# Kernel tuning notes

Hardware: AMD Instinct MI355X
Metric: run time of the kernel (lower is better)

## Reference

```python
import jax, jax.numpy as jnp
import numpy as np

N = 50000      # nodes
E = 500000     # edges (includes N self-loops)
DIN = 512
DOUT = 256
NEG_SLOPE = 0.01  # torch nn.LeakyReLU default


def setup_inputs() -> dict:
    key = jax.random.key(0)
    k1, k2, k3, k4, k5 = jax.random.split(key, 5)
    x = jax.random.normal(k1, (N, DIN), dtype=jnp.float32)
    # xavier_normal_ with gain=1.414
    std_W = 1.414 * np.sqrt(2.0 / (DIN + DOUT))
    W = jax.random.normal(k2, (DIN, DOUT), dtype=jnp.float32) * std_W
    std_a = 1.414 * np.sqrt(2.0 / (1 + 2 * DOUT))
    a = jax.random.normal(k3, (2 * DOUT,), dtype=jnp.float32) * std_a
    # first N edges are self-loops so every row-sum is nonzero
    loops = jnp.arange(N, dtype=jnp.int32)
    edge_src = jnp.concatenate([loops, jax.random.randint(k4, (E - N,), 0, N, dtype=jnp.int32)])
    edge_dst = jnp.concatenate([loops, jax.random.randint(k5, (E - N,), 0, N, dtype=jnp.int32)])
    return {"x": x, "W": W, "a": a, "edge_src": edge_src, "edge_dst": edge_dst}


def reference(x, W, a, edge_src, edge_dst):
    n = x.shape[0]
    d = W.shape[1]
    h = x @ W  # [N, DOUT]
    # a . [h_src ; h_dst] decomposed per-node, then gathered per-edge
    s_src = h @ a[:d]   # [N]
    s_dst = h @ a[d:]   # [N]
    score = s_src[edge_src] + s_dst[edge_dst]          # [E]
    e = jnp.exp(-jax.nn.leaky_relu(score, NEG_SLOPE))  # [E]
    # sparse softmax denominator: spmm(edge, e, ones) == segment sum over src
    e_rowsum = jax.ops.segment_sum(e, edge_src, num_segments=n)            # [N]
    # numerator: spmm(edge, e, h) == sum_j e_ij * h_j per row i
    h_prime = jax.ops.segment_sum(e[:, None] * h[edge_dst], edge_src, num_segments=n)  # [N, DOUT]
    h_prime = h_prime / e_rowsum[:, None]
    return jax.nn.elu(h_prime)  # concat=True branch
```

## Files before the change

### kernel.cpp

```cpp
#include <hip/hip_runtime.h>
#include <math.h>

#define DIN 512
#define DOUT 256
#define NEG_SLOPE 0.01f

typedef __attribute__((ext_vector_type(8))) short bf16x8;
typedef __attribute__((ext_vector_type(4))) float f32x4;
typedef __attribute__((ext_vector_type(4))) unsigned int u32x4;

__device__ __forceinline__ unsigned short f2bf(float f) {
    unsigned int u = __float_as_uint(f);
    unsigned int r = (u + 0x7FFFu + ((u >> 16) & 1u)) >> 16;
    return (unsigned short)r;
}
__device__ __forceinline__ float bf2f(unsigned short u) {
    return __uint_as_float(((unsigned int)u) << 16);
}
__device__ __forceinline__ unsigned int cvtpk(float lo, float hi) {
    unsigned int r;
    asm("v_cvt_pk_bf16_f32 %0, %1, %2" : "=v"(r) : "v"(lo), "v"(hi));
    return r;
}

__global__ void prep(const float* __restrict__ W, unsigned short* __restrict__ Bp,
                     int* __restrict__ deg, float* __restrict__ s_src,
                     float* __restrict__ s_dst, int N) {
    int t = blockIdx.x * blockDim.x + threadIdx.x;
    if (t < (DIN / 32) * (DOUT / 16) * 64) {
        int lane = t & 63;
        int cg = (t >> 6) & 15;
        int ks = t >> 10;
        int l15 = lane & 15, g = lane >> 4;
        int col = cg * 16 + l15;
        int k0 = ks * 32 + g * 8;
        ushort4 lo, hi;
        lo.x = f2bf(W[(size_t)(k0 + 0) * DOUT + col]);
        lo.y = f2bf(W[(size_t)(k0 + 1) * DOUT + col]);
        lo.z = f2bf(W[(size_t)(k0 + 2) * DOUT + col]);
        lo.w = f2bf(W[(size_t)(k0 + 3) * DOUT + col]);
        hi.x = f2bf(W[(size_t)(k0 + 4) * DOUT + col]);
        hi.y = f2bf(W[(size_t)(k0 + 5) * DOUT + col]);
        hi.z = f2bf(W[(size_t)(k0 + 6) * DOUT + col]);
        hi.w = f2bf(W[(size_t)(k0 + 7) * DOUT + col]);
        *(ushort4*)(Bp + (size_t)t * 8) = lo;
        *(ushort4*)(Bp + (size_t)t * 8 + 4) = hi;
    }
    if (t < N) { deg[t] = 0; s_src[t] = 0.f; s_dst[t] = 0.f; }
}

__global__ __launch_bounds__(256, 4) void gemm_k(const float* __restrict__ x,
                                                 const unsigned short* __restrict__ Bp,
                                                 unsigned short* __restrict__ hb,
                                                 const float* __restrict__ av,
                                                 float* __restrict__ s_src,
                                                 float* __restrict__ s_dst, int M) {
    const int t = threadIdx.x;
    const int lane = t & 63;
    const int l15 = lane & 15;
    const int g = lane >> 4;
    const int wv = t >> 6;
    const int m0 = blockIdx.x * 32;

    f32x4 acc[2][4] = {};
    int r0 = min(m0 + l15, M - 1);
    int r1 = min(m0 + 16 + l15, M - 1);
    const float* pA0 = x + (size_t)r0 * DIN + g * 8;
    const float* pA1 = x + (size_t)r1 * DIN + g * 8;
    const unsigned short* pB = Bp + ((size_t)(wv * 4) * 64 + lane) * 8;

#pragma unroll 4
    for (int ks = 0; ks < DIN / 32; ++ks) {
        f32x4 v0 = *(const f32x4*)(pA0 + ks * 32);
        f32x4 v1 = *(const f32x4*)(pA0 + ks * 32 + 4);
        f32x4 w0 = *(const f32x4*)(pA1 + ks * 32);
        f32x4 w1 = *(const f32x4*)(pA1 + ks * 32 + 4);
        u32x4 p;
        p.x = cvtpk(v0.x, v0.y); p.y = cvtpk(v0.z, v0.w);
        p.z = cvtpk(v1.x, v1.y); p.w = cvtpk(v1.z, v1.w);
        bf16x8 afr0 = *(bf16x8*)&p;
        u32x4 q;
        q.x = cvtpk(w0.x, w0.y); q.y = cvtpk(w0.z, w0.w);
        q.z = cvtpk(w1.x, w1.y); q.w = cvtpk(w1.z, w1.w);
        bf16x8 afr1 = *(bf16x8*)&q;
#pragma unroll
        for (int cf = 0; cf < 4; ++cf) {
            bf16x8 bfr = *(const bf16x8*)(pB + ((size_t)(ks * 16 + cf) * 64) * 8);
            acc[0][cf] = __builtin_amdgcn_mfma_f32_16x16x32_bf16(afr0, bfr, acc[0][cf], 0, 0, 0);
            acc[1][cf] = __builtin_amdgcn_mfma_f32_16x16x32_bf16(afr1, bfr, acc[1][cf], 0, 0, 0);
        }
    }

    float as_[4], ad_[4];
#pragma unroll
    for (int cf = 0; cf < 4; ++cf) {
        int col = wv * 64 + cf * 16 + l15;
        as_[cf] = av[col];
        ad_[cf] = av[DOUT + col];
    }
#pragma unroll
    for (int rf = 0; rf < 2; ++rf) {
#pragma unroll
        for (int j = 0; j < 4; ++j) {
            int row = m0 + rf * 16 + g * 4 + j;
            float ps = 0.f, pd = 0.f;
#pragma unroll
            for (int cf = 0; cf < 4; ++cf) {
                float v = acc[rf][cf][j];
                ps += v * as_[cf];
                pd += v * ad_[cf];
            }
#pragma unroll
            for (int off = 1; off < 16; off <<= 1) {
                ps += __shfl_xor(ps, off);
                pd += __shfl_xor(pd, off);
            }
            if (row < M) {
#pragma unroll
                for (int cf = 0; cf < 4; ++cf)
                    hb[(size_t)row * DOUT + wv * 64 + cf * 16 + l15] = f2bf(acc[rf][cf][j]);
                if (l15 == 0) {
                    atomicAdd(&s_src[row], ps);
                    atomicAdd(&s_dst[row], pd);
                }
            }
        }
    }
}

__global__ void hist_k(const int* __restrict__ src, int* __restrict__ deg, int E) {
    int i = blockIdx.x * blockDim.x + threadIdx.x;
    if (i < E) atomicAdd(&deg[src[i]], 1);
}

__global__ __launch_bounds__(256) void block_sum(const int* __restrict__ deg, int* __restrict__ bsum, int N) {
    __shared__ int wsum[4];
    int b = blockIdx.x, t = threadIdx.x;
    int idx = b * 1024 + t * 4;
    int s = 0;
    if (idx + 3 < N) {
        int4 v = *(const int4*)(deg + idx);
        s = v.x + v.y + v.z + v.w;
    } else {
        for (int i = 0; i < 4; i++) if (idx + i < N) s += deg[idx + i];
    }
#pragma unroll
    for (int off = 32; off > 0; off >>= 1) s += __shfl_xor(s, off);
    if ((t & 63) == 0) wsum[t >> 6] = s;
    __syncthreads();
    if (t == 0) bsum[b] = wsum[0] + wsum[1] + wsum[2] + wsum[3];
}

__global__ void scan_tops(const int* __restrict__ bsum, int* __restrict__ boff,
                          int* __restrict__ rowptr, int nb, int N, int E) {
    int t = threadIdx.x;
    int v = (t < nb) ? bsum[t] : 0;
    int x = v;
#pragma unroll
    for (int off = 1; off < 64; off <<= 1) {
        int y = __shfl_up(x, off);
        if (t >= off) x += y;
    }
    if (t < nb) boff[t] = x - v;
    if (t == 0) rowptr[N] = E;
}

__global__ __launch_bounds__(256) void scan_blk(const int* __restrict__ deg, const int* __restrict__ boff,
                                                int* __restrict__ rowptr, int* __restrict__ cursor, int N) {
    __shared__ int wsum[4];
    int b = blockIdx.x, t = threadIdx.x;
    int idx = b * 1024 + t * 4;
    int v0 = 0, v1 = 0, v2 = 0, v3 = 0;
    if (idx + 3 < N) {
        int4 v = *(const int4*)(deg + idx);
        v0 = v.x; v1 = v.y; v2 = v.z; v3 = v.w;
    } else if (idx < N) {
        v0 = deg[idx];
        if (idx + 1 < N) v1 = deg[idx + 1];
        if (idx + 2 < N) v2 = deg[idx + 2];
    }
    int s = v0 + v1 + v2 + v3;
    int lane = t & 63, wid = t >> 6;
    int x = s;
#pragma unroll
    for (int off = 1; off < 64; off <<= 1) {
        int y = __shfl_up(x, off);
        if (lane >= off) x += y;
    }
    if (lane == 63) wsum[wid] = x;
    __syncthreads();
    int add = boff[b];
    for (int ww = 0; ww < wid; ++ww) add += wsum[ww];
    int e0 = add + x - s;
    int e1 = e0 + v0, e2 = e1 + v1, e3 = e2 + v2;
    if (idx < N)     { rowptr[idx] = e0;     cursor[idx] = e0; }
    if (idx + 1 < N) { rowptr[idx + 1] = e1; cursor[idx + 1] = e1; }
    if (idx + 2 < N) { rowptr[idx + 2] = e2; cursor[idx + 2] = e2; }
    if (idx + 3 < N) { rowptr[idx + 3] = e3; cursor[idx + 3] = e3; }
}

__global__ void edge_k(const int* __restrict__ src, const int* __restrict__ dst,
                       const float* __restrict__ s_src, const float* __restrict__ s_dst,
                       int* __restrict__ cursor, int2* __restrict__ csr, int E) {
    int i = blockIdx.x * blockDim.x + threadIdx.x;
    if (i >= E) return;
    int s = src[i], d = dst[i];
    float sc = s_src[s] + s_dst[d];
    float lrv = sc > 0.f ? sc : NEG_SLOPE * sc;
    float ev = __expf(-lrv);
    int pos = atomicAdd(&cursor[s], 1);
    csr[pos] = make_int2(d, __float_as_int(ev));
}

__global__ __launch_bounds__(256) void gather_k(const unsigned short* __restrict__ hb,
                                                const int* __restrict__ rowptr,
                                                const int2* __restrict__ csr,
                                                float* __restrict__ out, int N) {
    int gt = blockIdx.x * blockDim.x + threadIdx.x;
    int w = gt >> 6;
    int lane = threadIdx.x & 63;
    if (w >= N) return;
    int s0 = rowptr[w], s1 = rowptr[w + 1];
    float a0 = 0.f, a1 = 0.f, a2 = 0.f, a3 = 0.f, rs = 0.f;
    for (int base = s0; base < s1; base += 64) {
        int cnt = min(64, s1 - base);
        int dv = 0; float ev = 0.f;
        if (lane < cnt) {
            int2 p = csr[base + lane];
            dv = p.x; ev = __int_as_float(p.y);
        }
        int jj = 0;
        for (; jj + 4 <= cnt; jj += 4) {
            int d0 = __shfl(dv, jj), d1 = __shfl(dv, jj + 1), d2 = __shfl(dv, jj + 2), d3 = __shfl(dv, jj + 3);
            float e0 = __shfl(ev, jj), e1 = __shfl(ev, jj + 1), e2 = __shfl(ev, jj + 2), e3 = __shfl(ev, jj + 3);
            ushort4 h0 = *(const ushort4*)(hb + (size_t)d0 * DOUT + lane * 4);
            ushort4 h1 = *(const ushort4*)(hb + (size_t)d1 * DOUT + lane * 4);
            ushort4 h2 = *(const ushort4*)(hb + (size_t)d2 * DOUT + lane * 4);
            ushort4 h3 = *(const ushort4*)(hb + (size_t)d3 * DOUT + lane * 4);
            a0 += e0 * bf2f(h0.x) + e1 * bf2f(h1.x) + e2 * bf2f(h2.x) + e3 * bf2f(h3.x);
            a1 += e0 * bf2f(h0.y) + e1 * bf2f(h1.y) + e2 * bf2f(h2.y) + e3 * bf2f(h3.y);
            a2 += e0 * bf2f(h0.z) + e1 * bf2f(h1.z) + e2 * bf2f(h2.z) + e3 * bf2f(h3.z);
            a3 += e0 * bf2f(h0.w) + e1 * bf2f(h1.w) + e2 * bf2f(h2.w) + e3 * bf2f(h3.w);
            rs += e0 + e1 + e2 + e3;
        }
        for (; jj < cnt; ++jj) {
            int d0 = __shfl(dv, jj);
            float e0 = __shfl(ev, jj);
            ushort4 h0 = *(const ushort4*)(hb + (size_t)d0 * DOUT + lane * 4);
            a0 += e0 * bf2f(h0.x);
            a1 += e0 * bf2f(h0.y);
            a2 += e0 * bf2f(h0.z);
            a3 += e0 * bf2f(h0.w);
            rs += e0;
        }
    }
    float inv = 1.f / rs;
    float4 v;
    v.x = a0 * inv; v.y = a1 * inv; v.z = a2 * inv; v.w = a3 * inv;
    v.x = v.x > 0.f ? v.x : __expf(v.x) - 1.f;
    v.y = v.y > 0.f ? v.y : __expf(v.y) - 1.f;
    v.z = v.z > 0.f ? v.z : __expf(v.z) - 1.f;
    v.w = v.w > 0.f ? v.w : __expf(v.w) - 1.f;
    *(float4*)(out + (size_t)w * DOUT + lane * 4) = v;
}

extern "C" void kernel_launch(void* const* d_in, const int* in_sizes, int n_in,
                              void* d_out, int out_size, void* d_ws, size_t ws_size,
                              hipStream_t stream) {
    const float* x = (const float*)d_in[0];
    const float* W = (const float*)d_in[1];
    const float* a = (const float*)d_in[2];
    const int* edge_src = (const int*)d_in[3];
    const int* edge_dst = (const int*)d_in[4];

    const int N = in_sizes[0] / DIN;
    const int E = in_sizes[3];
    const int nb = (N + 1023) / 1024;

    char* ws = (char*)d_ws;
    size_t off = 0;
    auto alloc = [&](size_t bytes) {
        void* p = ws + off;
        off += (bytes + 15) & ~(size_t)15;
        return p;
    };
    unsigned short* hb = (unsigned short*)alloc((size_t)N * DOUT * 2);
    unsigned short* Bp = (unsigned short*)alloc((size_t)DIN * DOUT * 2);
    int* rowptr = (int*)alloc((size_t)(N + 1) * 4);
    int* deg = (int*)alloc((size_t)N * 4);
    int* cursor = (int*)alloc((size_t)N * 4);
    float* s_src = (float*)alloc((size_t)N * 4);
    float* s_dst = (float*)alloc((size_t)N * 4);
    int2* csr = (int2*)alloc((size_t)E * 8);
    int* bsum = (int*)alloc((size_t)nb * 4);
    int* boff = (int*)alloc((size_t)nb * 4);
    (void)ws_size;

    float* out = (float*)d_out;

    prep<<<(N + 255) / 256, 256, 0, stream>>>(W, Bp, deg, s_src, s_dst, N);
    hist_k<<<(E + 255) / 256, 256, 0, stream>>>(edge_src, deg, E);
    gemm_k<<<(N + 31) / 32, 256, 0, stream>>>(x, Bp, hb, a, s_src, s_dst, N);
    block_sum<<<nb, 256, 0, stream>>>(deg, bsum, N);
    scan_tops<<<1, 64, 0, stream>>>(bsum, boff, rowptr, nb, N, E);
    scan_blk<<<nb, 256, 0, stream>>>(deg, boff, rowptr, cursor, N);
    edge_k<<<(E + 255) / 256, 256, 0, stream>>>(edge_src, edge_dst, s_src, s_dst,
                                                cursor, csr, E);
    gather_k<<<(N + 3) / 4, 256, 0, stream>>>(hb, rowptr, csr, out, N);
}
```

Measured before the change: 178.7 us.

## Give each GEMM wave full output width over 16 rows with bulk A prefetch

The GEMM tiling changes from four waves sharing 32 rows, each owning 64 output columns, to each wave owning 16 rows across all 256 columns. Each block now covers 64 rows. Each wave reads its x rows exactly once, loaded in two large batches of sixteen 16-byte loads, so the second half streams in while the first half's MFMAs run. This removes the 4x redundant reads of x across waves but reads all of the packed W per wave. It also raises register use (16 accumulators plus 16 raw vectors), and the occupancy hint is dropped from launch bounds.

```diff
diff --git a/kernel.cpp b/kernel.cpp
--- a/kernel.cpp
+++ b/kernel.cpp
@@ -49,80 +49,106 @@
     if (t < N) { deg[t] = 0; s_src[t] = 0.f; s_dst[t] = 0.f; }
 }
 
-__global__ __launch_bounds__(256, 4) void gemm_k(const float* __restrict__ x,
-                                                 const unsigned short* __restrict__ Bp,
-                                                 unsigned short* __restrict__ hb,
-                                                 const float* __restrict__ av,
-                                                 float* __restrict__ s_src,
-                                                 float* __restrict__ s_dst, int M) {
+__global__ __launch_bounds__(256) void gemm_k(const float* __restrict__ x,
+                                              const unsigned short* __restrict__ Bp,
+                                              unsigned short* __restrict__ hb,
+                                              const float* __restrict__ av,
+                                              float* __restrict__ s_src,
+                                              float* __restrict__ s_dst, int M) {
     const int t = threadIdx.x;
     const int lane = t & 63;
     const int l15 = lane & 15;
     const int g = lane >> 4;
     const int wv = t >> 6;
-    const int m0 = blockIdx.x * 32;
-
-    f32x4 acc[2][4] = {};
-    int r0 = min(m0 + l15, M - 1);
-    int r1 = min(m0 + 16 + l15, M - 1);
-    const float* pA0 = x + (size_t)r0 * DIN + g * 8;
-    const float* pA1 = x + (size_t)r1 * DIN + g * 8;
-    const unsigned short* pB = Bp + ((size_t)(wv * 4) * 64 + lane) * 8;
-
-#pragma unroll 4
-    for (int ks = 0; ks < DIN / 32; ++ks) {
-        f32x4 v0 = *(const f32x4*)(pA0 + ks * 32);
-        f32x4 v1 = *(const f32x4*)(pA0 + ks * 32 + 4);
-        f32x4 w0 = *(const f32x4*)(pA1 + ks * 32);
-        f32x4 w1 = *(const f32x4*)(pA1 + ks * 32 + 4);
+    const int m0 = blockIdx.x * 64 + wv * 16;
+
+    int r = min(m0 + l15, M - 1);
+    const float* pA = x + (size_t)r * DIN + g * 8;
+    const unsigned short* pB = Bp + (size_t)lane * 8;
+
+    f32x4 acc[16] = {};
+    bf16x8 afr[8];
+
+    {
+        f32x4 raw[16];
+#pragma unroll
+        for (int i = 0; i < 8; ++i) {
+            raw[2 * i] = *(const f32x4*)(pA + i * 32);
+            raw[2 * i + 1] = *(const f32x4*)(pA + i * 32 + 4);
+        }
+#pragma unroll
+        for (int i = 0; i < 8; ++i) {
+            u32x4 p;
+            p.x = cvtpk(raw[2 * i].x, raw[2 * i].y);
+            p.y = cvtpk(raw[2 * i].z, raw[2 * i].w);
+            p.z = cvtpk(raw[2 * i + 1].x, raw[2 * i + 1].y);
+            p.w = cvtpk(raw[2 * i + 1].z, raw[2 * i + 1].w);
+            afr[i] = *(bf16x8*)&p;
+        }
+    }
+    f32x4 raw2[16];
+#pragma unroll
+    for (int i = 0; i < 8; ++i) {
+        raw2[2 * i] = *(const f32x4*)(pA + 256 + i * 32);
+        raw2[2 * i + 1] = *(const f32x4*)(pA + 256 + i * 32 + 4);
+    }
+#pragma unroll
+    for (int ks = 0; ks < 8; ++ks) {
+        const unsigned short* pBks = pB + (size_t)ks * 16 * 512;
+#pragma unroll
+        for (int cg = 0; cg < 16; ++cg) {
+            bf16x8 bfr = *(const bf16x8*)(pBks + (size_t)cg * 512);
+            acc[cg] = __builtin_amdgcn_mfma_f32_16x16x32_bf16(afr[ks], bfr, acc[cg], 0, 0, 0);
+        }
+    }
+#pragma unroll
+    for (int i = 0; i < 8; ++i) {
         u32x4 p;
-        p.x = cvtpk(v0.x, v0.y); p.y = cvtpk(v0.z, v0.w);
-        p.z = cvtpk(v1.x, v1.y); p.w = cvtpk(v1.z, v1.w);
-        bf16x8 afr0 = *(bf16x8*)&p;
-        u32x4 q;
-        q.x = cvtpk(w0.x, w0.y); q.y = cvtpk(w0.z, w0.w);
-        q.z = cvtpk(w1.x, w1.y); q.w = cvtpk(w1.z, w1.w);
-        bf16x8 afr1 = *(bf16x8*)&q;
-#pragma unroll
-        for (int cf = 0; cf < 4; ++cf) {
-            bf16x8 bfr = *(const bf16x8*)(pB + ((size_t)(ks * 16 + cf) * 64) * 8);
-            acc[0][cf] = __builtin_amdgcn_mfma_f32_16x16x32_bf16(afr0, bfr, acc[0][cf], 0, 0, 0);
-            acc[1][cf] = __builtin_amdgcn_mfma_f32_16x16x32_bf16(afr1, bfr, acc[1][cf], 0, 0, 0);
-        }
-    }
-
-    float as_[4], ad_[4];
-#pragma unroll
-    for (int cf = 0; cf < 4; ++cf) {
-        int col = wv * 64 + cf * 16 + l15;
-        as_[cf] = av[col];
-        ad_[cf] = av[DOUT + col];
-    }
-#pragma unroll
-    for (int rf = 0; rf < 2; ++rf) {
-#pragma unroll
-        for (int j = 0; j < 4; ++j) {
-            int row = m0 + rf * 16 + g * 4 + j;
-            float ps = 0.f, pd = 0.f;
-#pragma unroll
-            for (int cf = 0; cf < 4; ++cf) {
-                float v = acc[rf][cf][j];
-                ps += v * as_[cf];
-                pd += v * ad_[cf];
-            }
-#pragma unroll
-            for (int off = 1; off < 16; off <<= 1) {
-                ps += __shfl_xor(ps, off);
-                pd += __shfl_xor(pd, off);
-            }
-            if (row < M) {
-#pragma unroll
-                for (int cf = 0; cf < 4; ++cf)
-                    hb[(size_t)row * DOUT + wv * 64 + cf * 16 + l15] = f2bf(acc[rf][cf][j]);
-                if (l15 == 0) {
-                    atomicAdd(&s_src[row], ps);
-                    atomicAdd(&s_dst[row], pd);
-                }
+        p.x = cvtpk(raw2[2 * i].x, raw2[2 * i].y);
+        p.y = cvtpk(raw2[2 * i].z, raw2[2 * i].w);
+        p.z = cvtpk(raw2[2 * i + 1].x, raw2[2 * i + 1].y);
+        p.w = cvtpk(raw2[2 * i + 1].z, raw2[2 * i + 1].w);
+        afr[i] = *(bf16x8*)&p;
+    }
+#pragma unroll
+    for (int ks = 0; ks < 8; ++ks) {
+        const unsigned short* pBks = pB + (size_t)(ks + 8) * 16 * 512;
+#pragma unroll
+        for (int cg = 0; cg < 16; ++cg) {
+            bf16x8 bfr = *(const bf16x8*)(pBks + (size_t)cg * 512);
+            acc[cg] = __builtin_amdgcn_mfma_f32_16x16x32_bf16(afr[ks], bfr, acc[cg], 0, 0, 0);
+        }
+    }
+
+    float as_[16], ad_[16];
+#pragma unroll
+    for (int cg = 0; cg < 16; ++cg) {
+        int col = cg * 16 + l15;
+        as_[cg] = av[col];
+        ad_[cg] = av[DOUT + col];
+    }
+#pragma unroll
+    for (int j = 0; j < 4; ++j) {
+        int row = m0 + g * 4 + j;
+        float ps = 0.f, pd = 0.f;
+#pragma unroll
+        for (int cg = 0; cg < 16; ++cg) {
+            float v = acc[cg][j];
+            ps += v * as_[cg];
+            pd += v * ad_[cg];
+        }
+#pragma unroll
+        for (int off = 1; off < 16; off <<= 1) {
+            ps += __shfl_xor(ps, off);
+            pd += __shfl_xor(pd, off);
+        }
+        if (row < M) {
+#pragma unroll
+            for (int cg = 0; cg < 16; ++cg)
+                hb[(size_t)row * DOUT + cg * 16 + l15] = f2bf(acc[cg][j]);
+            if (l15 == 0) {
+                atomicAdd(&s_src[row], ps);
+                atomicAdd(&s_dst[row], pd);
             }
         }
     }
@@ -300,7 +326,7 @@
 
     prep<<<(N + 255) / 256, 256, 0, stream>>>(W, Bp, deg, s_src, s_dst, N);
     hist_k<<<(E + 255) / 256, 256, 0, stream>>>(edge_src, deg, E);
-    gemm_k<<<(N + 31) / 32, 256, 0, stream>>>(x, Bp, hb, a, s_src, s_dst, N);
+    gemm_k<<<(N + 63) / 64, 256, 0, stream>>>(x, Bp, hb, a, s_src, s_dst, N);
     block_sum<<<nb, 256, 0, stream>>>(deg, bsum, N);
     scan_tops<<<1, 64, 0, stream>>>(bsum, boff, rowptr, nb, N, E);
     scan_blk<<<nb, 256, 0, stream>>>(deg, boff, rowptr, cursor, N);
```

After: 154.1 us. 1.16x faster.

## Compute full 32x256 output tile per single-wave block in GEMM

Applied to the files above, without the earlier changes.

The GEMM block shrinks from four waves, each covering 64 output columns, to one wave that covers all 256 columns for its 32 rows. Each x row chunk is now loaded and converted to bf16 once per block instead of four times, which removes redundant global reads and conversions. In exchange each wave holds 32 accumulator fragments, so register pressure rises and occupancy may drop. The loop is also fully unrolled.

```diff
diff --git a/kernel.cpp b/kernel.cpp
--- a/kernel.cpp
+++ b/kernel.cpp
@@ -49,54 +49,54 @@
     if (t < N) { deg[t] = 0; s_src[t] = 0.f; s_dst[t] = 0.f; }
 }
 
-__global__ __launch_bounds__(256, 4) void gemm_k(const float* __restrict__ x,
-                                                 const unsigned short* __restrict__ Bp,
-                                                 unsigned short* __restrict__ hb,
-                                                 const float* __restrict__ av,
-                                                 float* __restrict__ s_src,
-                                                 float* __restrict__ s_dst, int M) {
-    const int t = threadIdx.x;
-    const int lane = t & 63;
+__global__ __launch_bounds__(64, 2) void gemm_k(const float* __restrict__ x,
+                                                const unsigned short* __restrict__ Bp,
+                                                unsigned short* __restrict__ hb,
+                                                const float* __restrict__ av,
+                                                float* __restrict__ s_src,
+                                                float* __restrict__ s_dst, int M) {
+    const int lane = threadIdx.x;
     const int l15 = lane & 15;
     const int g = lane >> 4;
-    const int wv = t >> 6;
     const int m0 = blockIdx.x * 32;
 
-    f32x4 acc[2][4] = {};
     int r0 = min(m0 + l15, M - 1);
     int r1 = min(m0 + 16 + l15, M - 1);
     const float* pA0 = x + (size_t)r0 * DIN + g * 8;
     const float* pA1 = x + (size_t)r1 * DIN + g * 8;
-    const unsigned short* pB = Bp + ((size_t)(wv * 4) * 64 + lane) * 8;
-
-#pragma unroll 4
+    const unsigned short* pB = Bp + (size_t)lane * 8;
+
+    f32x4 acc[2][16] = {};
+
+#pragma unroll
     for (int ks = 0; ks < DIN / 32; ++ks) {
-        f32x4 v0 = *(const f32x4*)(pA0 + ks * 32);
-        f32x4 v1 = *(const f32x4*)(pA0 + ks * 32 + 4);
-        f32x4 w0 = *(const f32x4*)(pA1 + ks * 32);
-        f32x4 w1 = *(const f32x4*)(pA1 + ks * 32 + 4);
+        f32x4 a00 = *(const f32x4*)(pA0 + ks * 32);
+        f32x4 a01 = *(const f32x4*)(pA0 + ks * 32 + 4);
+        f32x4 a10 = *(const f32x4*)(pA1 + ks * 32);
+        f32x4 a11 = *(const f32x4*)(pA1 + ks * 32 + 4);
         u32x4 p;
-        p.x = cvtpk(v0.x, v0.y); p.y = cvtpk(v0.z, v0.w);
-        p.z = cvtpk(v1.x, v1.y); p.w = cvtpk(v1.z, v1.w);
-        bf16x8 afr0 = *(bf16x8*)&p;
+        p.x = cvtpk(a00.x, a00.y); p.y = cvtpk(a00.z, a00.w);
+        p.z = cvtpk(a01.x, a01.y); p.w = cvtpk(a01.z, a01.w);
+        bf16x8 af0 = *(bf16x8*)&p;
         u32x4 q;
-        q.x = cvtpk(w0.x, w0.y); q.y = cvtpk(w0.z, w0.w);
-        q.z = cvtpk(w1.x, w1.y); q.w = cvtpk(w1.z, w1.w);
-        bf16x8 afr1 = *(bf16x8*)&q;
-#pragma unroll
-        for (int cf = 0; cf < 4; ++cf) {
-            bf16x8 bfr = *(const bf16x8*)(pB + ((size_t)(ks * 16 + cf) * 64) * 8);
-            acc[0][cf] = __builtin_amdgcn_mfma_f32_16x16x32_bf16(afr0, bfr, acc[0][cf], 0, 0, 0);
-            acc[1][cf] = __builtin_amdgcn_mfma_f32_16x16x32_bf16(afr1, bfr, acc[1][cf], 0, 0, 0);
-        }
-    }
-
-    float as_[4], ad_[4];
-#pragma unroll
-    for (int cf = 0; cf < 4; ++cf) {
-        int col = wv * 64 + cf * 16 + l15;
-        as_[cf] = av[col];
-        ad_[cf] = av[DOUT + col];
+        q.x = cvtpk(a10.x, a10.y); q.y = cvtpk(a10.z, a10.w);
+        q.z = cvtpk(a11.x, a11.y); q.w = cvtpk(a11.z, a11.w);
+        bf16x8 af1 = *(bf16x8*)&q;
+        const unsigned short* pBks = pB + (size_t)ks * 16 * 512;
+#pragma unroll
+        for (int cg = 0; cg < 16; ++cg) {
+            bf16x8 bfr = *(const bf16x8*)(pBks + (size_t)cg * 512);
+            acc[0][cg] = __builtin_amdgcn_mfma_f32_16x16x32_bf16(af0, bfr, acc[0][cg], 0, 0, 0);
+            acc[1][cg] = __builtin_amdgcn_mfma_f32_16x16x32_bf16(af1, bfr, acc[1][cg], 0, 0, 0);
+        }
+    }
+
+    float as_[16], ad_[16];
+#pragma unroll
+    for (int cg = 0; cg < 16; ++cg) {
+        int col = cg * 16 + l15;
+        as_[cg] = av[col];
+        ad_[cg] = av[DOUT + col];
     }
 #pragma unroll
     for (int rf = 0; rf < 2; ++rf) {
@@ -105,10 +105,10 @@
             int row = m0 + rf * 16 + g * 4 + j;
             float ps = 0.f, pd = 0.f;
 #pragma unroll
-            for (int cf = 0; cf < 4; ++cf) {
-                float v = acc[rf][cf][j];
-                ps += v * as_[cf];
-                pd += v * ad_[cf];
+            for (int cg = 0; cg < 16; ++cg) {
+                float v = acc[rf][cg][j];
+                ps += v * as_[cg];
+                pd += v * ad_[cg];
             }
 #pragma unroll
             for (int off = 1; off < 16; off <<= 1) {
@@ -117,8 +117,8 @@
             }
             if (row < M) {
 #pragma unroll
-                for (int cf = 0; cf < 4; ++cf)
-                    hb[(size_t)row * DOUT + wv * 64 + cf * 16 + l15] = f2bf(acc[rf][cf][j]);
+                for (int cg = 0; cg < 16; ++cg)
+                    hb[(size_t)row * DOUT + cg * 16 + l15] = f2bf(acc[rf][cg][j]);
                 if (l15 == 0) {
                     atomicAdd(&s_src[row], ps);
                     atomicAdd(&s_dst[row], pd);
@@ -300,7 +300,7 @@
 
     prep<<<(N + 255) / 256, 256, 0, stream>>>(W, Bp, deg, s_src, s_dst, N);
     hist_k<<<(E + 255) / 256, 256, 0, stream>>>(edge_src, deg, E);
-    gemm_k<<<(N + 31) / 32, 256, 0, stream>>>(x, Bp, hb, a, s_src, s_dst, N);
+    gemm_k<<<(N + 31) / 32, 64, 0, stream>>>(x, Bp, hb, a, s_src, s_dst, N);
     block_sum<<<nb, 256, 0, stream>>>(deg, bsum, N);
     scan_tops<<<1, 64, 0, stream>>>(bsum, boff, rowptr, nb, N, E);
     scan_blk<<<nb, 256, 0, stream>>>(deg, boff, rowptr, cursor, N);
```

Result: faster. 149.2 us (-16.5%).
